# Kernel tuning notes

Hardware: AMD Instinct MI355X
Metric: run time of the kernel (lower is better)

Reference implementation:

```python
import jax, jax.numpy as jnp
import numpy as np

N_NODES = 50000


def gcn_conv_max(x, edge_index, edge_weight, W, b):
    """PyG GCNConv with aggr='max': gcn_norm (add self-loops, symmetric
    degree normalization), linear transform, gather-scale-scatter_max, bias."""
    n = x.shape[0]
    row, col = edge_index[0], edge_index[1]
    loop = jnp.arange(n)
    row = jnp.concatenate([row, loop])  # sources (incl. self-loops)
    col = jnp.concatenate([col, loop])  # targets
    ew = jnp.concatenate([edge_weight, jnp.ones((n,), x.dtype)])
    deg = jax.ops.segment_sum(ew, col, num_segments=n)
    dis = jnp.where(deg > 0, jax.lax.rsqrt(deg), jnp.zeros_like(deg))
    norm = dis[row] * ew * dis[col]  # [E+N]
    h = x @ W                         # [N, out]
    msg = norm[:, None] * h[row]      # gather + scale, [E+N, out]
    agg = jax.ops.segment_max(msg, col, num_segments=n)  # scatter-max
    return agg + b


def setup_inputs() -> dict:
    key = jax.random.key(0)
    ks = jax.random.split(key, 9)
    N, E = N_NODES, 1_600_000
    x = jax.random.normal(ks[0], (N, 5), dtype=jnp.float32)
    edge_index = jax.random.randint(ks[1], (2, E), 0, N, dtype=jnp.int64)
    edge_weight = jax.random.uniform(ks[2], (E,), dtype=jnp.float32)
    s1 = 1.0 / np.sqrt(5.0)
    s2 = 1.0 / np.sqrt(240.0)
    W1 = jax.random.uniform(ks[3], (5, 240), jnp.float32, -s1, s1)
    b1 = jnp.zeros((240,), jnp.float32)
    W2 = jax.random.uniform(ks[4], (240, 240), jnp.float32, -s2, s2)
    b2 = jnp.zeros((240,), jnp.float32)
    We = jax.random.uniform(ks[5], (240, 80), jnp.float32, -s2, s2)
    be = jnp.zeros((80,), jnp.float32)
    return {"x": x, "edge_index": edge_index, "edge_weight": edge_weight,
            "W1": W1, "b1": b1, "W2": W2, "b2": b2, "We": We, "be": be}


def reference(x, edge_index, edge_weight, W1, b1, W2, b2, We, be):
    h = gcn_conv_max(x, edge_index, edge_weight, W1, b1)
    h = jax.nn.relu(h)
    h = gcn_conv_max(h, edge_index, edge_weight, W2, b2)
    h = jax.nn.relu(h)
    return h @ We + be  # [N, 80]
```

## Files before the change

kernel.cpp:

```cpp
#include <hip/hip_runtime.h>
#include <cfloat>

#define HID 240

static inline size_t alignUp(size_t x, size_t a){ return (x + a - 1) / a * a; }

typedef __bf16 bf16x8 __attribute__((ext_vector_type(8)));
typedef unsigned short u16x8 __attribute__((ext_vector_type(8)));
typedef float  f32x16 __attribute__((ext_vector_type(16)));
typedef float  f32x4  __attribute__((ext_vector_type(4)));

__device__ __forceinline__ float b2f(unsigned short u){
    return __uint_as_float(((unsigned)u) << 16);
}
__device__ __forceinline__ unsigned short f2b_rne(float f){
    unsigned r = __float_as_uint(f);
    r += 0x7FFFu + ((r >> 16) & 1u);
    return (unsigned short)(r >> 16);
}
__device__ __forceinline__ float max3f(float a, float b, float c){
    return fmaxf(fmaxf(a, b), c);
}

__device__ __forceinline__ float vmax16(f32x16 a){
    float x0 = fmaxf(fmaxf(a[0],  a[1]),  a[2]);
    float x1 = fmaxf(fmaxf(a[3],  a[4]),  a[5]);
    float x2 = fmaxf(fmaxf(a[6],  a[7]),  a[8]);
    float x3 = fmaxf(fmaxf(a[9],  a[10]), a[11]);
    float x4 = fmaxf(fmaxf(a[12], a[13]), a[14]);
    float y0 = fmaxf(fmaxf(x0, x1), x2);
    float y1 = fmaxf(fmaxf(x3, x4), a[15]);
    return fmaxf(y0, y1);
}

__global__ void k_deg_prep(const int* __restrict__ col, const float* __restrict__ ew,
                           unsigned long long* __restrict__ pk, unsigned* __restrict__ rank,
                           int E, int ne, int N, int nb,
                           const float* __restrict__ x, float* __restrict__ xp,
                           const float* __restrict__ W1, unsigned short* __restrict__ W1f,
                           const float* __restrict__ W2, unsigned short* __restrict__ Bt2h,
                           unsigned short* __restrict__ Bt2l,
                           const float* __restrict__ We, unsigned short* __restrict__ Bt3h,
                           unsigned short* __restrict__ Bt3l){
    int b = blockIdx.x;
    int t = threadIdx.x;
    if (b < ne){
        int e = b * 256 + t;
        if (e < E){
            int c = col[e];
            unsigned q = __float2uint_rn(ew[e] * 1048576.0f);
            unsigned long long old = atomicAdd(&pk[c], (1ull << 40) | (unsigned long long)q);
            rank[e] = (unsigned)(old >> 40);
        }
        return;
    }
    int bb = b - ne;
    if (bb < nb){
        __shared__ float s[1280];
        int rbase = bb * 256;
        #pragma unroll
        for (int c = 0; c < 5; c++){
            int idx = rbase * 5 + t + 256 * c;
            s[t + 256 * c] = (idx < N * 5) ? x[idx] : 0.0f;
        }
        __syncthreads();
        #pragma unroll
        for (int c = 0; c < 8; c++){
            int pos = t + 256 * c;
            int r = pos >> 3, j = pos & 7;
            int grow = rbase + r;
            if (grow < N)
                xp[(size_t)grow * 8 + j] = (j < 5) ? s[r * 5 + j] : 0.0f;
        }
        return;
    }
    bb -= nb;
    if (bb < 32){
        int i = bb * 256 + t;
        if (i < 2 * 8 * 64 * 8){
            int k    = i & 7;
            int lane = (i >> 3) & 63;
            int j    = (i >> 9) & 7;
            int s2   = i >> 12;
            int lm = lane & 31, quad = lane >> 5;
            int kg = quad * 8 + k;
            int colm = 32 * j + lm;
            float v = (kg < 5 && colm < HID) ? W1[kg * HID + colm] : 0.0f;
            unsigned short hi = f2b_rne(v);
            W1f[i] = (s2 == 0) ? hi : f2b_rne(v - b2f(hi));
        }
        return;
    }
    bb -= 32;
    if (bb < 240){
        int i = bb * 256 + t;
        int n = i / HID, k = i - n * HID;
        float v = (n < HID) ? W2[(size_t)k * HID + n] : 0.0f;
        unsigned short hi = f2b_rne(v);
        Bt2h[i] = hi;
        Bt2l[i] = f2b_rne(v - b2f(hi));
        return;
    }
    bb -= 240;
    {
        int i = bb * 256 + t;
        if (i < 128 * HID){
            int n = i / HID, k = i - n * HID;
            float v = (n < 80) ? We[(size_t)k * 80 + n] : 0.0f;
            unsigned short hi = f2b_rne(v);
            Bt3h[i] = hi;
            Bt3l[i] = f2b_rne(v - b2f(hi));
        }
    }
}

__global__ void k_dis_bsum(const unsigned long long* __restrict__ pk,
                           float* __restrict__ dis, unsigned* __restrict__ cnt,
                           unsigned* __restrict__ bsum, int N){
    int b = blockIdx.x;
    int i = b * 256 + threadIdx.x;
    unsigned v = 0u;
    if (i < N){
        unsigned long long p = pk[i];
        unsigned c = (unsigned)(p >> 40);
        cnt[i] = c;
        float deg = 1.0f + (float)(p & 0xFFFFFFFFFFull) * (1.0f / 1048576.0f);
        dis[i] = rsqrtf(deg);
        v = (c + 32u) >> 5;
    }
    #pragma unroll
    for (int o = 32; o > 0; o >>= 1) v += __shfl_down(v, (unsigned)o, 64);
    __shared__ unsigned ws[4];
    int lane = threadIdx.x & 63, w = threadIdx.x >> 6;
    if (lane == 0) ws[w] = v;
    __syncthreads();
    if (threadIdx.x == 0) bsum[b] = ws[0] + ws[1] + ws[2] + ws[3];
}

__global__ void k_bscan(const unsigned* __restrict__ bsum, unsigned* __restrict__ boff,
                        unsigned* __restrict__ poff, int nb, int N){
    __shared__ unsigned s[256];
    int t = threadIdx.x;
    unsigned v = (t < nb) ? bsum[t] : 0u;
    s[t] = v;
    __syncthreads();
    for (int o = 1; o < 256; o <<= 1){
        unsigned u = (t >= o) ? s[t - o] : 0u;
        __syncthreads();
        s[t] += u;
        __syncthreads();
    }
    if (t < nb) boff[t] = s[t] - v;
    if (t == 0) poff[N] = 32u * s[nb - 1];
}

__global__ void k_offs_fill(const unsigned* __restrict__ cnt, const unsigned* __restrict__ boff,
                            const float* __restrict__ dis,
                            unsigned* __restrict__ poff, int2* __restrict__ sedge, int N){
    int b = blockIdx.x, t = threadIdx.x;
    int i = b * 256 + t;
    unsigned c = (i < N) ? cnt[i] : 0u;
    unsigned v = (i < N) ? ((c + 32u) >> 5) : 0u;
    int lane = t & 63, w = t >> 6;
    unsigned x = v;
    #pragma unroll
    for (int o = 1; o < 64; o <<= 1){
        unsigned u = __shfl_up(x, (unsigned)o, 64);
        if (lane >= o) x += u;
    }
    __shared__ unsigned ws[4];
    if (lane == 63) ws[w] = x;
    __syncthreads();
    unsigned wb = 0;
    if (w > 0) wb += ws[0];
    if (w > 1) wb += ws[1];
    if (w > 2) wb += ws[2];
    if (i < N){
        unsigned p = 32u * (boff[b] + wb + x - v);
        poff[i] = p;
        float dd = dis[i];
        int2 sv = make_int2(i, __float_as_int(dd * dd));
        sedge[p] = sv;
        unsigned s1 = p + 32u * v;
        for (unsigned s = p + 1u + c; s < s1; s++) sedge[s] = sv;
    }
}

__global__ void k_scatter(const int* __restrict__ row, const int* __restrict__ col,
                          const float* __restrict__ ew, const float* __restrict__ dis,
                          const unsigned* __restrict__ poff, const unsigned* __restrict__ rank,
                          int2* __restrict__ sedge, int E){
    int e = blockIdx.x * blockDim.x + threadIdx.x;
    if (e < E){
        int r = row[e], c = col[e];
        float nw = dis[r] * ew[e] * dis[c];
        unsigned p = poff[c] + 1u + rank[e];
        sedge[p] = make_int2(r, __float_as_int(nw));
    }
}

__global__ __launch_bounds__(256) void k_agg1m(const float* __restrict__ xp,
                                               const unsigned short* __restrict__ W1f,
                                               const unsigned* __restrict__ cnt,
                                               const unsigned* __restrict__ poff,
                                               const int2* __restrict__ sedge,
                                               const float* __restrict__ bias,
                                               float* __restrict__ out, int N, int nwaves){
    int wid  = blockIdx.x * 4 + (threadIdx.x >> 6);
    int lane = threadIdx.x & 63;
    int lm   = lane & 31;

    bf16x8 bh[8], bl[8];
    #pragma unroll
    for (int j = 0; j < 8; j++){
        bh[j] = *(const bf16x8*)(W1f + ((size_t)(0 * 8 + j) * 64 + lane) * 8);
        bl[j] = *(const bf16x8*)(W1f + ((size_t)(1 * 8 + j) * 64 + lane) * 8);
    }
    float bv[8];
    #pragma unroll
    for (int j = 0; j < 8; j++){
        int c = 32 * j + lm;
        bv[j] = (c < HID) ? bias[c] : 0.0f;
    }
    const f32x16 zv = {};

    for (int d = wid; d < N; d += nwaves){
        unsigned base = poff[d];
        unsigned nch  = (cnt[d] + 32u) >> 5;
        float m[8];
        #pragma unroll
        for (int j = 0; j < 8; j++) m[j] = -FLT_MAX;

        for (unsigned c = 0; c < nch; c++){
            u16x8 ahu = (u16x8)0, alu = (u16x8)0;
            if (lane < 32){
                int2 e = sedge[base + 32u * c + (unsigned)lm];
                float w = __int_as_float(e.y);
                const float4* xr = (const float4*)(xp + (size_t)e.x * 8);
                float4 x0 = xr[0], x1 = xr[1];
                float p[5] = {w * x0.x, w * x0.y, w * x0.z, w * x0.w, w * x1.x};
                #pragma unroll
                for (int k = 0; k < 5; k++){
                    unsigned short h = f2b_rne(p[k]);
                    ahu[k] = h;
                    alu[k] = f2b_rne(p[k] - b2f(h));
                }
            }
            bf16x8 ah = __builtin_bit_cast(bf16x8, ahu);
            bf16x8 al = __builtin_bit_cast(bf16x8, alu);
            #pragma unroll
            for (int j = 0; j < 8; j += 2){
                f32x16 a0 = __builtin_amdgcn_mfma_f32_32x32x16_bf16(ah, bh[j],     zv, 0, 0, 0);
                f32x16 a1 = __builtin_amdgcn_mfma_f32_32x32x16_bf16(ah, bh[j + 1], zv, 0, 0, 0);
                a0 = __builtin_amdgcn_mfma_f32_32x32x16_bf16(ah, bl[j],     a0, 0, 0, 0);
                a1 = __builtin_amdgcn_mfma_f32_32x32x16_bf16(ah, bl[j + 1], a1, 0, 0, 0);
                a0 = __builtin_amdgcn_mfma_f32_32x32x16_bf16(al, bh[j],     a0, 0, 0, 0);
                a1 = __builtin_amdgcn_mfma_f32_32x32x16_bf16(al, bh[j + 1], a1, 0, 0, 0);
                m[j]     = fmaxf(m[j],     vmax16(a0));
                m[j + 1] = fmaxf(m[j + 1], vmax16(a1));
            }
        }
        float o[8];
        #pragma unroll
        for (int j = 0; j < 8; j++){
            float other = __shfl_xor(m[j], 32, 64);
            o[j] = fmaxf(fmaxf(m[j], other) + bv[j], 0.0f);
        }
        if (lane < 32){
            float* orow = out + (size_t)d * HID;
            #pragma unroll
            for (int j = 0; j < 8; j++){
                int c = 32 * j + lm;
                if (c < HID) orow[c] = o[j];
            }
        }
    }
}

template <bool OB16>
__global__ __launch_bounds__(256) void k_gemm_mfma(const float* __restrict__ A,
                                                   const unsigned short* __restrict__ Bth,
                                                   const unsigned short* __restrict__ Btl,
                                                   const float* __restrict__ bias,
                                                   void* __restrict__ Cv,
                                                   int M, int Ncol, int Npad, int Cld){
    __shared__ unsigned short As_hi[64][24];
    __shared__ unsigned short As_lo[64][24];
    const int K = 240;
    int t = threadIdx.x;
    int wave = t >> 6, lane = t & 63;
    int m0 = blockIdx.x * 64;
    int n0 = wave * 64;
    bool wact = n0 < Npad;

    int lm   = lane & 31;
    int quad = lane >> 5;

    f32x16 acc[2][2] = {};

    for (int k0 = 0; k0 < K; k0 += 16){
        {
            int m = t >> 2, kq = (t & 3) * 4;
            float4 av = make_float4(0.f, 0.f, 0.f, 0.f);
            if (m0 + m < M) av = *(const float4*)(A + (size_t)(m0 + m) * K + k0 + kq);
            ushort4 hi, lo;
            hi.x = f2b_rne(av.x); lo.x = f2b_rne(av.x - b2f(hi.x));
            hi.y = f2b_rne(av.y); lo.y = f2b_rne(av.y - b2f(hi.y));
            hi.z = f2b_rne(av.z); lo.z = f2b_rne(av.z - b2f(hi.z));
            hi.w = f2b_rne(av.w); lo.w = f2b_rne(av.w - b2f(hi.w));
            *(ushort4*)&As_hi[m][kq] = hi;
            *(ushort4*)&As_lo[m][kq] = lo;
        }
        __syncthreads();
        if (wact){
            size_t bo0 = (size_t)(n0 + lm) * K + k0 + quad * 8;
            size_t bo1 = (size_t)(n0 + 32 + lm) * K + k0 + quad * 8;
            bf16x8 bh0 = *(const bf16x8*)(Bth + bo0);
            bf16x8 bl0 = *(const bf16x8*)(Btl + bo0);
            bf16x8 bh1 = *(const bf16x8*)(Bth + bo1);
            bf16x8 bl1 = *(const bf16x8*)(Btl + bo1);
            #pragma unroll
            for (int mh = 0; mh < 2; mh++){
                bf16x8 ah = *(const bf16x8*)&As_hi[32 * mh + lm][quad * 8];
                bf16x8 al = *(const bf16x8*)&As_lo[32 * mh + lm][quad * 8];
                acc[mh][0] = __builtin_amdgcn_mfma_f32_32x32x16_bf16(ah, bh0, acc[mh][0], 0, 0, 0);
                acc[mh][0] = __builtin_amdgcn_mfma_f32_32x32x16_bf16(ah, bl0, acc[mh][0], 0, 0, 0);
                acc[mh][0] = __builtin_amdgcn_mfma_f32_32x32x16_bf16(al, bh0, acc[mh][0], 0, 0, 0);
                acc[mh][1] = __builtin_amdgcn_mfma_f32_32x32x16_bf16(ah, bh1, acc[mh][1], 0, 0, 0);
                acc[mh][1] = __builtin_amdgcn_mfma_f32_32x32x16_bf16(ah, bl1, acc[mh][1], 0, 0, 0);
                acc[mh][1] = __builtin_amdgcn_mfma_f32_32x32x16_bf16(al, bh1, acc[mh][1], 0, 0, 0);
            }
        }
        __syncthreads();
    }

    if (!wact) return;
    #pragma unroll
    for (int mh = 0; mh < 2; mh++){
        #pragma unroll
        for (int h = 0; h < 2; h++){
            int n = n0 + 32 * h + lm;
            if (n >= Ncol) continue;
            float bvv = (!OB16 && bias) ? bias[n] : 0.0f;
            #pragma unroll
            for (int r = 0; r < 16; r++){
                int m = m0 + 32 * mh + (r & 3) + 8 * (r >> 2) + 4 * quad;
                if (m >= M) continue;
                float v = acc[mh][h][r];
                if (OB16){
                    ((unsigned short*)Cv)[(size_t)m * Cld + n] = f2b_rne(v);
                } else {
                    ((float*)Cv)[(size_t)m * Cld + n] = v + bvv;
                }
            }
        }
    }
}

__global__ __launch_bounds__(256) void k_aggb_f(const unsigned short* __restrict__ H2,
                                                const unsigned* __restrict__ cnt,
                                                const unsigned* __restrict__ poff,
                                                const int2* __restrict__ sedge,
                                                const float* __restrict__ bias,
                                                const unsigned short* __restrict__ Bt3h,
                                                const unsigned short* __restrict__ Bt3l,
                                                const float* __restrict__ be,
                                                float* __restrict__ out, int N){
    __shared__ unsigned short Ah[16][264];
    __shared__ unsigned short Al[16][264];

    int t    = threadIdx.x;
    int wid  = t >> 6;
    int lane = t & 63;
    int tbase = blockIdx.x * 16;

    for (int i = t; i < 16 * 24; i += 256){
        int r = i / 24, c = 240 + (i % 24);
        Ah[r][c] = 0;
        Al[r][c] = 0;
    }

    bool act = lane < 60;
    float4 bv = act ? ((const float4*)bias)[lane] : make_float4(0.f, 0.f, 0.f, 0.f);
    #pragma unroll
    for (int i = 0; i < 4; i++){
        int rowi = wid * 4 + i;
        int d = tbase + rowi;
        unsigned p0  = (d < N) ? poff[d] : 0u;
        unsigned ng8 = (d < N) ? ((cnt[d] + 8u) >> 3) : 0u;
        const int2* se = sedge + p0;

        float4 m = make_float4(-FLT_MAX, -FLT_MAX, -FLT_MAX, -FLT_MAX);
        for (unsigned it = 0; it < ng8; it++){
            int2 e0 = se[0], e1 = se[1], e2 = se[2], e3 = se[3];
            int2 e4 = se[4], e5 = se[5], e6 = se[6], e7 = se[7];
            se += 8;
            if (act){
                ushort4 g0 = ((const ushort4*)(H2 + ((size_t)(unsigned)e0.x << 8)))[lane];
                ushort4 g1 = ((const ushort4*)(H2 + ((size_t)(unsigned)e1.x << 8)))[lane];
                ushort4 g2 = ((const ushort4*)(H2 + ((size_t)(unsigned)e2.x << 8)))[lane];
                ushort4 g3 = ((const ushort4*)(H2 + ((size_t)(unsigned)e3.x << 8)))[lane];
                ushort4 g4 = ((const ushort4*)(H2 + ((size_t)(unsigned)e4.x << 8)))[lane];
                ushort4 g5 = ((const ushort4*)(H2 + ((size_t)(unsigned)e5.x << 8)))[lane];
                ushort4 g6 = ((const ushort4*)(H2 + ((size_t)(unsigned)e6.x << 8)))[lane];
                ushort4 g7 = ((const ushort4*)(H2 + ((size_t)(unsigned)e7.x << 8)))[lane];
                float w0 = __int_as_float(e0.y), w1 = __int_as_float(e1.y);
                float w2 = __int_as_float(e2.y), w3 = __int_as_float(e3.y);
                float w4 = __int_as_float(e4.y), w5 = __int_as_float(e5.y);
                float w6 = __int_as_float(e6.y), w7 = __int_as_float(e7.y);
                m.x = max3f(max3f(w0*b2f(g0.x), w1*b2f(g1.x), w2*b2f(g2.x)),
                            max3f(w3*b2f(g3.x), w4*b2f(g4.x), w5*b2f(g5.x)),
                            max3f(w6*b2f(g6.x), w7*b2f(g7.x), m.x));
                m.y = max3f(max3f(w0*b2f(g0.y), w1*b2f(g1.y), w2*b2f(g2.y)),
                            max3f(w3*b2f(g3.y), w4*b2f(g4.y), w5*b2f(g5.y)),
                            max3f(w6*b2f(g6.y), w7*b2f(g7.y), m.y));
                m.z = max3f(max3f(w0*b2f(g0.z), w1*b2f(g1.z), w2*b2f(g2.z)),
                            max3f(w3*b2f(g3.z), w4*b2f(g4.z), w5*b2f(g5.z)),
                            max3f(w6*b2f(g6.z), w7*b2f(g7.z), m.z));
                m.w = max3f(max3f(w0*b2f(g0.w), w1*b2f(g1.w), w2*b2f(g2.w)),
                            max3f(w3*b2f(g3.w), w4*b2f(g4.w), w5*b2f(g5.w)),
                            max3f(w6*b2f(g6.w), w7*b2f(g7.w), m.w));
            }
        }
        if (act && (d < N)){
            float o0 = fmaxf(m.x + bv.x, 0.0f);
            float o1 = fmaxf(m.y + bv.y, 0.0f);
            float o2 = fmaxf(m.z + bv.z, 0.0f);
            float o3 = fmaxf(m.w + bv.w, 0.0f);
            ushort4 hi, lo;
            hi.x = f2b_rne(o0); lo.x = f2b_rne(o0 - b2f(hi.x));
            hi.y = f2b_rne(o1); lo.y = f2b_rne(o1 - b2f(hi.y));
            hi.z = f2b_rne(o2); lo.z = f2b_rne(o2 - b2f(hi.z));
            hi.w = f2b_rne(o3); lo.w = f2b_rne(o3 - b2f(hi.w));
            *(ushort4*)&Ah[rowi][lane * 4] = hi;
            *(ushort4*)&Al[rowi][lane * 4] = lo;
        } else if (act){
            ushort4 z = make_ushort4(0, 0, 0, 0);
            *(ushort4*)&Ah[rowi][lane * 4] = z;
            *(ushort4*)&Al[rowi][lane * 4] = z;
        }
    }
    __syncthreads();

    int arow = lane & 15;
    int kgrp = (lane >> 4) * 8;
    for (int tile = wid; tile < 5; tile += 4){
        int n0 = tile * 16;
        int coln = n0 + (lane & 15);
        f32x4 acc = {};
        #pragma unroll
        for (int kk = 0; kk < 256; kk += 32){
            bf16x8 ah = *(const bf16x8*)&Ah[arow][kk + kgrp];
            bf16x8 al = *(const bf16x8*)&Al[arow][kk + kgrp];
            bf16x8 bh = *(const bf16x8*)(Bt3h + (size_t)coln * 240 + kk + kgrp);
            bf16x8 bl = *(const bf16x8*)(Bt3l + (size_t)coln * 240 + kk + kgrp);
            acc = __builtin_amdgcn_mfma_f32_16x16x32_bf16(ah, bh, acc, 0, 0, 0);
            acc = __builtin_amdgcn_mfma_f32_16x16x32_bf16(ah, bl, acc, 0, 0, 0);
            acc = __builtin_amdgcn_mfma_f32_16x16x32_bf16(al, bh, acc, 0, 0, 0);
        }
        float bev = be[coln];
        #pragma unroll
        for (int r = 0; r < 4; r++){
            int mrow = (lane >> 4) * 4 + r;
            int d2 = tbase + mrow;
            if (d2 < N)
                out[(size_t)d2 * 80 + coln] = acc[r] + bev;
        }
    }
}

extern "C" void kernel_launch(void* const* d_in, const int* in_sizes, int n_in,
                              void* d_out, int out_size, void* d_ws, size_t ws_size,
                              hipStream_t stream){
    const float* x  = (const float*)d_in[0];
    const int*   ei = (const int*)  d_in[1];
    const float* ew = (const float*)d_in[2];
    const float* W1 = (const float*)d_in[3];
    const float* b1 = (const float*)d_in[4];
    const float* W2 = (const float*)d_in[5];
    const float* b2 = (const float*)d_in[6];
    const float* We = (const float*)d_in[7];
    const float* be = (const float*)d_in[8];
    float* out = (float*)d_out;

    const int N = in_sizes[0] / 5;
    const int E = in_sizes[2];
    const int* row = ei;
    const int* col = ei + E;
    const int nb = (N + 255) / 256;

    char* w = (char*)d_ws;
    size_t o = 0;
    auto alloc = [&](size_t bytes) -> void* {
        void* p = w + o;
        o = alignUp(o + bytes, 256);
        return p;
    };
    unsigned long long* pk = (unsigned long long*) alloc((size_t)N * 8);
    float*          dis   = (float*)          alloc((size_t)N * 4);
    unsigned*       cnt   = (unsigned*)       alloc((size_t)N * 4);
    unsigned*       poff  = (unsigned*)       alloc((size_t)(N + 1) * 4);
    unsigned*       bsum  = (unsigned*)       alloc((size_t)nb * 4);
    unsigned*       boff  = (unsigned*)       alloc((size_t)nb * 4);
    unsigned*       rank  = (unsigned*)       alloc((size_t)E * 4);
    int2*           sedge = (int2*)           alloc(((size_t)E + 32u * N + 64u) * 8);
    float*          xp    = (float*)          alloc((size_t)N * 8 * 4);
    unsigned short* W1f   = (unsigned short*) alloc((size_t)2 * 8 * 64 * 8 * 2);
    unsigned short* Bt2h  = (unsigned short*) alloc((size_t)256 * HID * 2);
    unsigned short* Bt2l  = (unsigned short*) alloc((size_t)256 * HID * 2);
    unsigned short* Bt3h  = (unsigned short*) alloc((size_t)128 * HID * 2);
    unsigned short* Bt3l  = (unsigned short*) alloc((size_t)128 * HID * 2);
    unsigned short* bufH2 = (unsigned short*) alloc((size_t)N * 256 * 2);
    float*          bufB  = (float*)          alloc((size_t)N * HID * 4);
    (void)ws_size; (void)n_in; (void)out_size;

    int ne = (E + 255) / 256;

    hipMemsetAsync(pk, 0, (size_t)N * 8, stream);
    k_deg_prep <<<ne + nb + 32 + 240 + 120, 256, 0, stream>>>(col, ew, pk, rank, E, ne, N, nb,
                                                              x, xp, W1, W1f,
                                                              W2, Bt2h, Bt2l,
                                                              We, Bt3h, Bt3l);
    k_dis_bsum <<<nb, 256, 0, stream>>>(pk, dis, cnt, bsum, N);
    k_bscan    <<<1, 256, 0, stream>>>(bsum, boff, poff, nb, N);
    k_offs_fill<<<nb, 256, 0, stream>>>(cnt, boff, dis, poff, sedge, N);
    k_scatter  <<<ne, 256, 0, stream>>>(row, col, ew, dis, poff, rank, sedge, E);

    const int a1blocks = 1536;
    k_agg1m<<<a1blocks, 256, 0, stream>>>(xp, W1f, cnt, poff, sedge, b1, bufB, N, a1blocks * 4);

    int gm = (N + 63) / 64;
    k_gemm_mfma<true><<<gm, 256, 0, stream>>>(bufB, Bt2h, Bt2l, nullptr, bufH2, N, HID, 256, 256);

    k_aggb_f<<<(N + 15) / 16, 256, 0, stream>>>(bufH2, cnt, poff, sedge, b2,
                                                Bt3h, Bt3l, be, out, N);
}
```

Before: 452.0 us.

## Give each wave its own rows in fused aggregation+GEMM to drop block barrier

The final aggregation kernel now has each wave own four destination rows in a private LDS slice. The block-wide __syncthreads becomes a wave-local LDS wait plus a scheduling barrier, so a wave can start its output GEMM as soon as its own gathers finish, without waiting on slower waves. In exchange each wave runs all five output tiles on 16-row MFMAs where only four rows are distinct. That multiplies MFMA work and reads of the weight matrix from global memory by roughly four per wave, and only a quarter of the lanes write results.

```diff
diff --git a/kernel.cpp b/kernel.cpp
--- a/kernel.cpp
+++ b/kernel.cpp
@@ -366,26 +366,20 @@
                                                 const unsigned short* __restrict__ Bt3l,
                                                 const float* __restrict__ be,
                                                 float* __restrict__ out, int N){
-    __shared__ unsigned short Ah[16][264];
-    __shared__ unsigned short Al[16][264];
-
-    int t    = threadIdx.x;
-    int wid  = t >> 6;
-    int lane = t & 63;
-    int tbase = blockIdx.x * 16;
-
-    for (int i = t; i < 16 * 24; i += 256){
-        int r = i / 24, c = 240 + (i % 24);
-        Ah[r][c] = 0;
-        Al[r][c] = 0;
-    }
+    __shared__ unsigned short Ah[4][4][264];
+    __shared__ unsigned short Al[4][4][264];
+
+    int t     = threadIdx.x;
+    int wid   = t >> 6;
+    int lane  = t & 63;
+    int tbase = blockIdx.x * 16 + wid * 4;
 
     bool act = lane < 60;
     float4 bv = act ? ((const float4*)bias)[lane] : make_float4(0.f, 0.f, 0.f, 0.f);
+
     #pragma unroll
     for (int i = 0; i < 4; i++){
-        int rowi = wid * 4 + i;
-        int d = tbase + rowi;
+        int d = tbase + i;
         unsigned p0  = (d < N) ? poff[d] : 0u;
         unsigned ng8 = (d < N) ? ((cnt[d] + 8u) >> 3) : 0u;
         const int2* se = sedge + p0;
@@ -422,49 +416,50 @@
                             max3f(w6*b2f(g6.w), w7*b2f(g7.w), m.w));
             }
         }
+        ushort4 hi = make_ushort4(0, 0, 0, 0);
+        ushort4 lo = make_ushort4(0, 0, 0, 0);
         if (act && (d < N)){
             float o0 = fmaxf(m.x + bv.x, 0.0f);
             float o1 = fmaxf(m.y + bv.y, 0.0f);
             float o2 = fmaxf(m.z + bv.z, 0.0f);
             float o3 = fmaxf(m.w + bv.w, 0.0f);
-            ushort4 hi, lo;
             hi.x = f2b_rne(o0); lo.x = f2b_rne(o0 - b2f(hi.x));
             hi.y = f2b_rne(o1); lo.y = f2b_rne(o1 - b2f(hi.y));
             hi.z = f2b_rne(o2); lo.z = f2b_rne(o2 - b2f(hi.z));
             hi.w = f2b_rne(o3); lo.w = f2b_rne(o3 - b2f(hi.w));
-            *(ushort4*)&Ah[rowi][lane * 4] = hi;
-            *(ushort4*)&Al[rowi][lane * 4] = lo;
-        } else if (act){
-            ushort4 z = make_ushort4(0, 0, 0, 0);
-            *(ushort4*)&Ah[rowi][lane * 4] = z;
-            *(ushort4*)&Al[rowi][lane * 4] = z;
-        }
-    }
-    __syncthreads();
+        }
+        *(ushort4*)&Ah[wid][i][lane * 4] = hi;
+        *(ushort4*)&Al[wid][i][lane * 4] = lo;
+    }
+
+    asm volatile("s_waitcnt lgkmcnt(0)" ::: "memory");
+    __builtin_amdgcn_sched_barrier(0);
 
     int arow = lane & 15;
+    int asel = arow & 3;
     int kgrp = (lane >> 4) * 8;
-    for (int tile = wid; tile < 5; tile += 4){
-        int n0 = tile * 16;
-        int coln = n0 + (lane & 15);
+    #pragma unroll
+    for (int tile = 0; tile < 5; tile++){
+        int coln = tile * 16 + arow;
         f32x4 acc = {};
         #pragma unroll
         for (int kk = 0; kk < 256; kk += 32){
-            bf16x8 ah = *(const bf16x8*)&Ah[arow][kk + kgrp];
-            bf16x8 al = *(const bf16x8*)&Al[arow][kk + kgrp];
+            bf16x8 ah = *(const bf16x8*)&Ah[wid][asel][kk + kgrp];
+            bf16x8 al = *(const bf16x8*)&Al[wid][asel][kk + kgrp];
             bf16x8 bh = *(const bf16x8*)(Bt3h + (size_t)coln * 240 + kk + kgrp);
             bf16x8 bl = *(const bf16x8*)(Bt3l + (size_t)coln * 240 + kk + kgrp);
             acc = __builtin_amdgcn_mfma_f32_16x16x32_bf16(ah, bh, acc, 0, 0, 0);
             acc = __builtin_amdgcn_mfma_f32_16x16x32_bf16(ah, bl, acc, 0, 0, 0);
             acc = __builtin_amdgcn_mfma_f32_16x16x32_bf16(al, bh, acc, 0, 0, 0);
         }
-        float bev = be[coln];
-        #pragma unroll
-        for (int r = 0; r < 4; r++){
-            int mrow = (lane >> 4) * 4 + r;
-            int d2 = tbase + mrow;
-            if (d2 < N)
-                out[(size_t)d2 * 80 + coln] = acc[r] + bev;
+        if ((lane >> 4) == 0){
+            float bev = be[coln];
+            #pragma unroll
+            for (int r = 0; r < 4; r++){
+                int d2 = tbase + r;
+                if (d2 < N)
+                    out[(size_t)d2 * 80 + coln] = acc[r] + bev;
+            }
         }
     }
 }
```

After: 506.2 us. 1.12x slower.

## Sort nodes by in-degree to balance warp work in final aggregation

Applied to the files above, without the earlier changes.

Adds a counting sort of nodes by in-degree (histogram, scan, atomic placement) and has the final aggregation kernel process nodes in that order. Rows sharing a block then have similar edge counts, which is meant to cut intra-block load imbalance and idle waves. Output rows are written back through the permutation. The cost is three extra small kernel launches, an indirection per row, scattered output stores, and less locality in the offset and edge reads.

```diff
diff --git a/kernel.cpp b/kernel.cpp
--- a/kernel.cpp
+++ b/kernel.cpp
@@ -196,6 +196,34 @@
         float nw = dis[r] * ew[e] * dis[c];
         unsigned p = poff[c] + 1u + rank[e];
         sedge[p] = make_int2(r, __float_as_int(nw));
+    }
+}
+
+__global__ void k_hist(const unsigned* __restrict__ cnt, unsigned* __restrict__ hist, int N){
+    int i = blockIdx.x * 256 + threadIdx.x;
+    if (i < N) atomicAdd(&hist[min(cnt[i], 255u)], 1u);
+}
+__global__ void k_hscan(const unsigned* __restrict__ hist, unsigned* __restrict__ hoff){
+    __shared__ unsigned s[256];
+    int t = threadIdx.x;
+    unsigned v = hist[t];
+    s[t] = v;
+    __syncthreads();
+    for (int o = 1; o < 256; o <<= 1){
+        unsigned u = (t >= o) ? s[t - o] : 0u;
+        __syncthreads();
+        s[t] += u;
+        __syncthreads();
+    }
+    hoff[t] = s[t] - v;
+}
+__global__ void k_place(const unsigned* __restrict__ cnt, unsigned* __restrict__ hoff,
+                        unsigned* __restrict__ ord, int N){
+    int i = blockIdx.x * 256 + threadIdx.x;
+    if (i < N){
+        unsigned b = min(cnt[i], 255u);
+        unsigned pos = atomicAdd(&hoff[b], 1u);
+        ord[pos] = (unsigned)i;
     }
 }
 
@@ -365,6 +393,7 @@
                                                 const unsigned short* __restrict__ Bt3h,
                                                 const unsigned short* __restrict__ Bt3l,
                                                 const float* __restrict__ be,
+                                                const unsigned* __restrict__ ord,
                                                 float* __restrict__ out, int N){
     __shared__ unsigned short Ah[16][264];
     __shared__ unsigned short Al[16][264];
@@ -385,7 +414,8 @@
     #pragma unroll
     for (int i = 0; i < 4; i++){
         int rowi = wid * 4 + i;
-        int d = tbase + rowi;
+        int gi = tbase + rowi;
+        int d = (gi < N) ? (int)ord[gi] : N;
         unsigned p0  = (d < N) ? poff[d] : 0u;
         unsigned ng8 = (d < N) ? ((cnt[d] + 8u) >> 3) : 0u;
         const int2* se = sedge + p0;
@@ -445,8 +475,7 @@
     int arow = lane & 15;
     int kgrp = (lane >> 4) * 8;
     for (int tile = wid; tile < 5; tile += 4){
-        int n0 = tile * 16;
-        int coln = n0 + (lane & 15);
+        int coln = tile * 16 + (lane & 15);
         f32x4 acc = {};
         #pragma unroll
         for (int kk = 0; kk < 256; kk += 32){
@@ -462,9 +491,9 @@
         #pragma unroll
         for (int r = 0; r < 4; r++){
             int mrow = (lane >> 4) * 4 + r;
-            int d2 = tbase + mrow;
-            if (d2 < N)
-                out[(size_t)d2 * 80 + coln] = acc[r] + bev;
+            int gi2 = tbase + mrow;
+            if (gi2 < N)
+                out[(size_t)ord[gi2] * 80 + coln] = acc[r] + bev;
         }
     }
 }
@@ -512,11 +541,15 @@
     unsigned short* Bt3l  = (unsigned short*) alloc((size_t)128 * HID * 2);
     unsigned short* bufH2 = (unsigned short*) alloc((size_t)N * 256 * 2);
     float*          bufB  = (float*)          alloc((size_t)N * HID * 4);
+    unsigned*       hist  = (unsigned*)       alloc(256 * 4);
+    unsigned*       hoff  = (unsigned*)       alloc(256 * 4);
+    unsigned*       ord   = (unsigned*)       alloc((size_t)N * 4);
     (void)ws_size; (void)n_in; (void)out_size;
 
     int ne = (E + 255) / 256;
 
     hipMemsetAsync(pk, 0, (size_t)N * 8, stream);
+    hipMemsetAsync(hist, 0, 256 * 4, stream);
     k_deg_prep <<<ne + nb + 32 + 240 + 120, 256, 0, stream>>>(col, ew, pk, rank, E, ne, N, nb,
                                                               x, xp, W1, W1f,
                                                               W2, Bt2h, Bt2l,
@@ -526,6 +559,10 @@
     k_offs_fill<<<nb, 256, 0, stream>>>(cnt, boff, dis, poff, sedge, N);
     k_scatter  <<<ne, 256, 0, stream>>>(row, col, ew, dis, poff, rank, sedge, E);
 
+    k_hist <<<nb, 256, 0, stream>>>(cnt, hist, N);
+    k_hscan<<<1, 256, 0, stream>>>(hist, hoff);
+    k_place<<<nb, 256, 0, stream>>>(cnt, hoff, ord, N);
+
     const int a1blocks = 1536;
     k_agg1m<<<a1blocks, 256, 0, stream>>>(xp, W1f, cnt, poff, sedge, b1, bufB, N, a1blocks * 4);
 
@@ -533,5 +570,5 @@
     k_gemm_mfma<true><<<gm, 256, 0, stream>>>(bufB, Bt2h, Bt2l, nullptr, bufH2, N, HID, 256, 256);
 
     k_aggb_f<<<(N + 15) / 16, 256, 0, stream>>>(bufH2, cnt, poff, sedge, b2,
-                                                Bt3h, Bt3l, be, out, N);
-}
+                                                Bt3h, Bt3l, be, ord, out, N);
+}
```

New measurement: 651.4 us. 1.44x slower.
